# Optimization experiments

Measured on AMD Instinct MI355X. Metric: run time of the kernel, lower is better.

The kernel has to match this reference:

```python
import jax, jax.numpy as jnp
import numpy as np

N_HEAD, D_MODEL, D_K, D_V = 16, 1024, 64, 64
B, S = 2, 2048


def setup_inputs() -> dict:
    key = jax.random.key(0)
    ks = jax.random.split(key, 8)
    xn = lambda k, shp: jax.random.normal(k, shp, dtype=jnp.float32)
    # xavier-normal-ish init for projection params
    std_qk = float(np.sqrt(2.0 / (D_MODEL + D_K)))
    std_v = float(np.sqrt(2.0 / (D_MODEL + D_V)))
    std_p = float(np.sqrt(2.0 / (N_HEAD * D_V + D_MODEL)))
    return {
        "q": xn(ks[0], (B, S, D_MODEL)),
        "k": xn(ks[1], (B, S, D_MODEL)),
        "v": xn(ks[2], (B, S, D_MODEL)),
        "w_qs": xn(ks[3], (N_HEAD, D_MODEL, D_K)) * std_qk,
        "w_ks": xn(ks[4], (N_HEAD, D_MODEL, D_K)) * std_qk,
        "w_vs": xn(ks[5], (N_HEAD, D_MODEL, D_V)) * std_v,
        "proj_w": xn(ks[6], (D_MODEL, N_HEAD * D_V)) * std_p,  # torch Linear weight (out, in)
        "proj_b": jnp.zeros((D_MODEL,), dtype=jnp.float32),
    }


def reference(q, k, v, w_qs, w_ks, w_vs, proj_w, proj_b):
    b, len_q, d_model = q.shape
    len_k = k.shape[1]
    temper = jnp.sqrt(jnp.asarray(d_model, q.dtype))  # NOTE: sqrt(d_model), not sqrt(d_k)
    # per-head projections (head-major, matching q.repeat(n_head,1,1) layout)
    qs = jnp.einsum('bqd,hdk->hbqk', q, w_qs)  # (H,B,Sq,Dk)
    ks = jnp.einsum('bsd,hdk->hbsk', k, w_ks)
    vs = jnp.einsum('bsd,hdv->hbsv', v, w_vs)
    att = jax.nn.softmax(jnp.einsum('hbqk,hbsk->hbqs', qs, ks) / temper, axis=-1)
    # dropout is identity in eval mode
    out = jnp.einsum('hbqs,hbsv->hbqv', att, vs)  # (H,B,Sq,Dv)
    # concat heads along feature dim in head order -> (B,Sq,H*Dv)
    out = jnp.transpose(out, (1, 2, 0, 3)).reshape(b, len_q, -1)
    out = out @ proj_w.T + proj_b
    attns = att.reshape(-1, len_q, len_k)  # (H*B, Sq, Sk) as in original
    return out, attns
```

## Files before the change

kernel.cpp:

```cpp
#include <hip/hip_runtime.h>
#include <hip/hip_bf16.h>
#include <math.h>


typedef __attribute__((ext_vector_type(8))) short short8;
typedef __attribute__((ext_vector_type(4))) float f32x4;
typedef __attribute__((ext_vector_type(4))) unsigned short ushort4v;

#define MFMA16(a, b, c) __builtin_amdgcn_mfma_f32_16x16x32_bf16(a, b, c, 0, 0, 0)
#define EXP2F(x) __builtin_amdgcn_exp2f(x)
#define LOG2F(x) __builtin_amdgcn_logf(x)

#define TILE_BARRIER(N) \
  asm volatile("s_waitcnt vmcnt(" #N ")\n\ts_barrier" ::: "memory")

static __device__ __forceinline__ unsigned short f2bf(float x) {
  unsigned int u = __float_as_uint(x);
  u += 0x7fffu + ((u >> 16) & 1u);
  return (unsigned short)(u >> 16);
}
static __device__ __forceinline__ unsigned int pack2bf(float a, float b) {
  return (unsigned int)f2bf(a) | ((unsigned int)f2bf(b) << 16);
}

static __device__ __forceinline__ void gload16(const unsigned short* g, unsigned short* l) {
  __builtin_amdgcn_global_load_lds(
      (const __attribute__((address_space(1))) unsigned int*)g,
      (__attribute__((address_space(3))) unsigned int*)l, 16, 0, 0);
}

__global__ void k_cvt_all(const float* __restrict__ q, const float* __restrict__ k,
                          const float* __restrict__ v, const float* __restrict__ pw,
                          unsigned short* __restrict__ qb, unsigned short* __restrict__ kb,
                          unsigned short* __restrict__ vb, unsigned short* __restrict__ pwb) {
  const int i = blockIdx.x * blockDim.x + threadIdx.x;
  const int N1 = 1048576;
  const float* s;
  unsigned short* d;
  int off;
  if (i < N1) { s = q; d = qb; off = i; }
  else if (i < 2 * N1) { s = k; d = kb; off = i - N1; }
  else if (i < 3 * N1) { s = v; d = vb; off = i - 2 * N1; }
  else { s = pw; d = pwb; off = i - 3 * N1; }
  float4 vv = reinterpret_cast<const float4*>(s)[off];
  ushort4v o;
  o.x = f2bf(vv.x); o.y = f2bf(vv.y); o.z = f2bf(vv.z); o.w = f2bf(vv.w);
  reinterpret_cast<ushort4v*>(d)[off] = o;
}

__global__ __launch_bounds__(256) void k_wt2(
    const float* __restrict__ s0, const float* __restrict__ s1, const float* __restrict__ s2,
    unsigned short* __restrict__ d0, unsigned short* __restrict__ d1,
    unsigned short* __restrict__ d2) {
  __shared__ float t[64][65];
  const int z = blockIdx.z;
  const float* __restrict__ s = (z == 0) ? s0 : ((z == 1) ? s1 : s2);
  unsigned short* __restrict__ d = (z == 0) ? d0 : ((z == 1) ? d1 : d2);
  const float wscale = (z == 0) ? 0.04508422002778011f : 1.0f;
  const int tid = threadIdx.x;
  const int h = blockIdx.y;
  const int dd0 = blockIdx.x * 64;
  const float* sp = s + ((size_t)h << 16);
  unsigned short* dp = d + ((size_t)h << 16);
#pragma unroll
  for (int it = 0; it < 16; ++it) {
    int dd = it * 4 + (tid >> 6);
    t[dd][tid & 63] = sp[(size_t)(dd0 + dd) * 64 + (tid & 63)];
  }
  __syncthreads();
#pragma unroll
  for (int it = 0; it < 16; ++it) {
    int kk = it * 4 + (tid >> 6);
    int dd = tid & 63;
    dp[(size_t)kk * 1024 + dd0 + dd] = f2bf(t[dd][kk] * wscale);
  }
}

__global__ __launch_bounds__(256, 3) void k_proj(
    const unsigned short* __restrict__ qb, const unsigned short* __restrict__ kb,
    const unsigned short* __restrict__ vb,
    const unsigned short* __restrict__ wqt, const unsigned short* __restrict__ wkt,
    const unsigned short* __restrict__ wvt,
    unsigned short* __restrict__ qs, unsigned short* __restrict__ ks,
    unsigned short* __restrict__ vst) {
  __shared__ unsigned short lA[2][4][128][8];
  __shared__ unsigned short lB[2][4][128][8];

  const int mode = blockIdx.z;
  const unsigned short* __restrict__ A = (mode == 0) ? qb : ((mode == 1) ? kb : vb);
  const unsigned short* __restrict__ W = (mode == 0) ? wqt : ((mode == 1) ? wkt : wvt);

  const int tid = threadIdx.x;
  const int wv = tid >> 6, lane = tid & 63, lq = lane & 15, g = lane >> 4;
  const int wr = wv >> 1, wc = wv & 1;
  const int m0 = blockIdx.x * 128;
  const int n0 = blockIdx.y * 128;

  const int rowm = tid & 127, kg = tid >> 7;
  const unsigned short* srcA = A + (size_t)(m0 + rowm) * 1024 + kg * 8;
  const unsigned short* srcB = W + (size_t)(n0 + rowm) * 1024 + kg * 8;
  unsigned short* dstA = &lA[0][0][0][0] + tid * 8;
  unsigned short* dstB = &lB[0][0][0][0] + tid * 8;

#define STAGE(bf, kc)                                       \
  do {                                                      \
    gload16(srcA + (kc), dstA + (bf)*4096);                 \
    gload16(srcA + (kc) + 16, dstA + (bf)*4096 + 2048);     \
    gload16(srcB + (kc), dstB + (bf)*4096);                 \
    gload16(srcB + (kc) + 16, dstB + (bf)*4096 + 2048);     \
  } while (0)

  f32x4 acc[4][4];
#pragma unroll
  for (int i = 0; i < 4; ++i)
#pragma unroll
    for (int j = 0; j < 4; ++j) acc[i][j] = (f32x4){0.f, 0.f, 0.f, 0.f};

  STAGE(0, 0);
  __syncthreads();
  for (int t = 0; t < 32; ++t) {
    const int buf = t & 1;
    if (t < 31) STAGE(buf ^ 1, (t + 1) * 32);
    short8 a[4], b[4];
#pragma unroll
    for (int i = 0; i < 4; ++i)
      a[i] = *reinterpret_cast<const short8*>(&lA[buf][g][wr * 64 + i * 16 + lq][0]);
#pragma unroll
    for (int j = 0; j < 4; ++j)
      b[j] = *reinterpret_cast<const short8*>(&lB[buf][g][wc * 64 + j * 16 + lq][0]);
#pragma unroll
    for (int i = 0; i < 4; ++i)
#pragma unroll
      for (int j = 0; j < 4; ++j) acc[i][j] = MFMA16(a[i], b[j], acc[i][j]);
    __syncthreads();
  }
#undef STAGE

#pragma unroll
  for (int i = 0; i < 4; ++i) {
#pragma unroll
    for (int j = 0; j < 4; ++j) {
      const int n = n0 + wc * 64 + j * 16 + lq;
      const int h = n >> 6, dk = n & 63;
#pragma unroll
      for (int r = 0; r < 4; ++r) {
        const int m = m0 + wr * 64 + i * 16 + g * 4 + r;
        const int b_ = m >> 11, sq = m & 2047;
        const unsigned short val = f2bf(acc[i][j][r]);
        if (mode == 0)
          qs[(((size_t)h * 2 + b_) * 2048 + sq) * 64 + dk] = val;
        else if (mode == 1)
          ks[(((size_t)h * 2 + b_) * 2048 + sq) * 64 + dk] = val;
        else
          vst[(((size_t)h * 2 + b_) * 64 + dk) * 2048 + sq] = val;
      }
    }
  }
}

__global__ __launch_bounds__(256, 2) void k_attn1(
    const unsigned short* __restrict__ qs, const unsigned short* __restrict__ ks,
    float* __restrict__ cf) {
  __shared__ unsigned short lk[2][4096];

  const int tid = threadIdx.x;
  const int wv = tid >> 6, lane = tid & 63, lq = lane & 15, g = lane >> 4;
  const int bid = blockIdx.x;
  const int xcd = bid & 7, j = bid >> 3;
  const int hb = xcd * 4 + (j & 3);
  const int qblk = j >> 2;
  const int q0 = qblk * 128 + wv * 32;

  const unsigned short* __restrict__ Q = qs + (size_t)hb * 2048 * 64;
  const unsigned short* __restrict__ K = ks + (size_t)hb * 2048 * 64;

  short8 bq[2][2];
#pragma unroll
  for (int s = 0; s < 2; ++s) {
    const size_t qr = (size_t)(q0 + s * 16 + lq) * 64;
    bq[s][0] = *reinterpret_cast<const short8*>(Q + qr + g * 8);
    bq[s][1] = *reinterpret_cast<const short8*>(Q + qr + 32 + g * 8);
  }

  const int srow = tid >> 3;
  const int scg = (tid & 7) ^ (srow & 7);
  const unsigned short* Ks0 = K + (size_t)srow * 64 + scg * 8;
  const unsigned short* Ks1 = K + (size_t)(srow + 32) * 64 + scg * 8;

#define STAGE_K(bf, kt0)                                   \
  do {                                                     \
    gload16(Ks0 + (size_t)(kt0) * 64, &lk[bf][tid * 8]);   \
    gload16(Ks1 + (size_t)(kt0) * 64, &lk[bf][(tid + 256) * 8]); \
  } while (0)

  float lrun[2] = {0.f, 0.f};
  STAGE_K(0, 0);
  TILE_BARRIER(0);
  for (int t = 0; t < 32; ++t) {
    const int buf = t & 1;
    if (t < 31) STAGE_K(buf ^ 1, (t + 1) * 64);
#pragma unroll
    for (int sub = 0; sub < 4; ++sub) {
      const int row = sub * 16 + lq;
      const int c0 = g ^ (row & 7);
      const unsigned short* lp = &lk[buf][row * 64];
      short8 ka0 = *reinterpret_cast<const short8*>(lp + c0 * 8);
      short8 ka1 = *reinterpret_cast<const short8*>(lp + (c0 ^ 4) * 8);
#pragma unroll
      for (int s = 0; s < 2; ++s) {
        f32x4 sa = (f32x4){0.f, 0.f, 0.f, 0.f};
        sa = MFMA16(ka0, bq[s][0], sa);
        sa = MFMA16(ka1, bq[s][1], sa);
        lrun[s] += (EXP2F(sa[0]) + EXP2F(sa[1])) + (EXP2F(sa[2]) + EXP2F(sa[3]));
      }
    }
    TILE_BARRIER(0);
  }
#pragma unroll
  for (int s = 0; s < 2; ++s) {
    float lc = lrun[s] + __shfl_xor(lrun[s], 16);
    lc += __shfl_xor(lc, 32);
    if (g == 0) cf[hb * 2048 + q0 + s * 16 + lq] = LOG2F(lc);
  }
#undef STAGE_K
}

__global__ __launch_bounds__(256, 2) void k_attn2(
    const unsigned short* __restrict__ qs, const unsigned short* __restrict__ ks,
    const unsigned short* __restrict__ vst, const float* __restrict__ cf,
    float* __restrict__ attns, unsigned short* __restrict__ att_out) {
  __shared__ unsigned short lk[2][4096];
  __shared__ unsigned short lv[2][4096];
  __shared__ unsigned char pscr[4][2][2048];

  const int tid = threadIdx.x;
  const int wv = tid >> 6, lane = tid & 63, lq = lane & 15, g = lane >> 4;
  const int bid = blockIdx.x;
  const int xcd = bid & 7, j = bid >> 3;
  const int hb = xcd * 4 + (j & 3);
  const int qblk = j >> 2;
  const int q0 = qblk * 128 + wv * 32;

  const unsigned short* __restrict__ Q = qs + (size_t)hb * 2048 * 64;
  const unsigned short* __restrict__ K = ks + (size_t)hb * 2048 * 64;
  const unsigned short* __restrict__ V = vst + (size_t)hb * 64 * 2048;

  short8 bq[2][2];
  float cfin[2];
#pragma unroll
  for (int s = 0; s < 2; ++s) {
    const size_t qr = (size_t)(q0 + s * 16 + lq) * 64;
    bq[s][0] = *reinterpret_cast<const short8*>(Q + qr + g * 8);
    bq[s][1] = *reinterpret_cast<const short8*>(Q + qr + 32 + g * 8);
    cfin[s] = cf[hb * 2048 + q0 + s * 16 + lq];
  }

  const int srow = tid >> 3;
  const int scg = (tid & 7) ^ (srow & 7);
  const unsigned short* Ks0 = K + (size_t)srow * 64 + scg * 8;
  const unsigned short* Ks1 = K + (size_t)(srow + 32) * 64 + scg * 8;
  const unsigned short* Vs0 = V + (size_t)srow * 2048 + scg * 8;
  const unsigned short* Vs1 = V + (size_t)(srow + 32) * 2048 + scg * 8;

#define STAGE_K(bf, kt0)                                   \
  do {                                                     \
    gload16(Ks0 + (size_t)(kt0) * 64, &lk[bf][tid * 8]);   \
    gload16(Ks1 + (size_t)(kt0) * 64, &lk[bf][(tid + 256) * 8]); \
  } while (0)
#define STAGE_V(bf, kt0)                                   \
  do {                                                     \
    gload16(Vs0 + (kt0), &lv[bf][tid * 8]);                \
    gload16(Vs1 + (kt0), &lv[bf][(tid + 256) * 8]);        \
  } while (0)

  f32x4 oacc[2][4];
#pragma unroll
  for (int s = 0; s < 2; ++s)
#pragma unroll
    for (int db = 0; db < 4; ++db) oacc[s][db] = (f32x4){0.f, 0.f, 0.f, 0.f};

  float* __restrict__ atile = attns + ((size_t)hb * 2048 + q0) * 2048;
  unsigned char* __restrict__ P0 = &pscr[wv][0][0];
  unsigned char* __restrict__ P1 = &pscr[wv][1][0];

  STAGE_K(0, 0);
  STAGE_V(0, 0);
  TILE_BARRIER(0);
  for (int t = 0; t < 32; ++t) {
    const int buf = t & 1;
    if (t < 31) {
      STAGE_K(buf ^ 1, (t + 1) * 64);
      STAGE_V(buf ^ 1, (t + 1) * 64);
    }
#pragma unroll
    for (int sub = 0; sub < 4; ++sub) {
      const int row = sub * 16 + lq;
      const int c0 = g ^ (row & 7);
      const unsigned short* lp = &lk[buf][row * 64];
      short8 ka0 = *reinterpret_cast<const short8*>(lp + c0 * 8);
      short8 ka1 = *reinterpret_cast<const short8*>(lp + (c0 ^ 4) * 8);
      const int cw = ((sub * 2 + (g >> 1)) ^ (lq & 7)) * 16 + (g & 1) * 8;
#pragma unroll
      for (int s = 0; s < 2; ++s) {
        f32x4 sa = (f32x4){0.f, 0.f, 0.f, 0.f};
        sa = MFMA16(ka0, bq[s][0], sa);
        sa = MFMA16(ka1, bq[s][1], sa);
        uint2 pr;
        pr.x = pack2bf(EXP2F(sa[0] - cfin[s]), EXP2F(sa[1] - cfin[s]));
        pr.y = pack2bf(EXP2F(sa[2] - cfin[s]), EXP2F(sa[3] - cfin[s]));
        *reinterpret_cast<uint2*>((s ? P1 : P0) + lq * 128 + cw) = pr;
      }
    }
#pragma unroll
    for (int s = 0; s < 2; ++s) {
      const unsigned char* Ps = s ? P1 : P0;
#pragma unroll
      for (int st = 0; st < 4; ++st) {
        const int rr = st * 4 + g;
        const int cr = ((lq >> 1) ^ (rr & 7)) * 16 + (lq & 1) * 8;
        const uint2 w = *reinterpret_cast<const uint2*>(Ps + rr * 128 + cr);
        f32x4 f4;
        f4[0] = __uint_as_float(w.x << 16);
        f4[1] = __uint_as_float(w.x & 0xffff0000u);
        f4[2] = __uint_as_float(w.y << 16);
        f4[3] = __uint_as_float(w.y & 0xffff0000u);
        float* dst = atile + (size_t)(s * 16 + rr) * 2048 + t * 64 + lq * 4;
        __builtin_nontemporal_store(f4, reinterpret_cast<f32x4*>(dst));
      }
    }
#pragma unroll
    for (int ch = 0; ch < 2; ++ch) {
      const int cp = ((ch * 4 + g) ^ (lq & 7)) * 16;
      short8 pb0 = *reinterpret_cast<const short8*>(P0 + lq * 128 + cp);
      short8 pb1 = *reinterpret_cast<const short8*>(P1 + lq * 128 + cp);
#pragma unroll
      for (int db = 0; db < 4; ++db) {
        const int row = db * 16 + lq;
        const int cv = (ch * 4 + g) ^ (row & 7);
        short8 va = *reinterpret_cast<const short8*>(&lv[buf][row * 64 + cv * 8]);
        oacc[0][db] = MFMA16(va, pb0, oacc[0][db]);
        oacc[1][db] = MFMA16(va, pb1, oacc[1][db]);
      }
    }
    if (t < 31) TILE_BARRIER(8);
  }

  const int h = hb >> 1, b_ = hb & 1;
#pragma unroll
  for (int s = 0; s < 2; ++s) {
    unsigned short* __restrict__ aob =
        att_out + ((size_t)(b_ * 2048 + q0 + s * 16 + lq)) * 1024 + h * 64;
#pragma unroll
    for (int db = 0; db < 4; ++db)
#pragma unroll
      for (int r = 0; r < 4; ++r)
        aob[db * 16 + g * 4 + r] = f2bf(oacc[s][db][r]);
  }
#undef STAGE_K
#undef STAGE_V
}

__global__ __launch_bounds__(256, 2) void k_oproj(
    const unsigned short* __restrict__ ao, const unsigned short* __restrict__ pw,
    const float* __restrict__ pb, float* __restrict__ out) {
  __shared__ unsigned short lA[2][4][64][8];
  __shared__ unsigned short lB[2][4][128][8];

  const int tid = threadIdx.x;
  const int wv = tid >> 6, lane = tid & 63, lq = lane & 15, g = lane >> 4;
  const int wr = wv >> 1, wc = wv & 1;
  const int m0 = blockIdx.x * 64;
  const int n0 = blockIdx.y * 128;

  const int rowa = tid & 63, kga = tid >> 6;
  const unsigned short* srcA = ao + (size_t)(m0 + rowa) * 1024 + kga * 8;
  unsigned short* dstA = &lA[0][0][0][0] + tid * 8;
  const int rowb = tid & 127, kgb = tid >> 7;
  const unsigned short* srcB = pw + (size_t)(n0 + rowb) * 1024 + kgb * 8;
  unsigned short* dstB = &lB[0][0][0][0] + tid * 8;

#define STAGE(bf, kc)                                       \
  do {                                                      \
    gload16(srcA + (kc), dstA + (bf)*2048);                 \
    gload16(srcB + (kc), dstB + (bf)*4096);                 \
    gload16(srcB + (kc) + 16, dstB + (bf)*4096 + 2048);     \
  } while (0)

  f32x4 acc[2][4];
#pragma unroll
  for (int i = 0; i < 2; ++i)
#pragma unroll
    for (int j = 0; j < 4; ++j) acc[i][j] = (f32x4){0.f, 0.f, 0.f, 0.f};

  STAGE(0, 0);
  __syncthreads();
  for (int t = 0; t < 32; ++t) {
    const int buf = t & 1;
    if (t < 31) STAGE(buf ^ 1, (t + 1) * 32);
    short8 a[2], b[4];
#pragma unroll
    for (int i = 0; i < 2; ++i)
      a[i] = *reinterpret_cast<const short8*>(&lA[buf][g][wr * 32 + i * 16 + lq][0]);
#pragma unroll
    for (int j = 0; j < 4; ++j)
      b[j] = *reinterpret_cast<const short8*>(&lB[buf][g][wc * 64 + j * 16 + lq][0]);
#pragma unroll
    for (int i = 0; i < 2; ++i)
#pragma unroll
      for (int j = 0; j < 4; ++j) acc[i][j] = MFMA16(a[i], b[j], acc[i][j]);
    __syncthreads();
  }
#undef STAGE

#pragma unroll
  for (int i = 0; i < 2; ++i) {
#pragma unroll
    for (int j = 0; j < 4; ++j) {
      const int n = n0 + wc * 64 + j * 16 + lq;
      const float bias = pb[n];
#pragma unroll
      for (int r = 0; r < 4; ++r) {
        const int m = m0 + wr * 32 + i * 16 + g * 4 + r;
        out[(size_t)m * 1024 + n] = acc[i][j][r] + bias;
      }
    }
  }
}

extern "C" void kernel_launch(void* const* d_in, const int* in_sizes, int n_in,
                              void* d_out, int out_size, void* d_ws, size_t ws_size,
                              hipStream_t stream) {
  const float* q = (const float*)d_in[0];
  const float* k = (const float*)d_in[1];
  const float* v = (const float*)d_in[2];
  const float* w_qs = (const float*)d_in[3];
  const float* w_ks = (const float*)d_in[4];
  const float* w_vs = (const float*)d_in[5];
  const float* proj_w = (const float*)d_in[6];
  const float* proj_b = (const float*)d_in[7];

  float* out = (float*)d_out;
  float* attns = out + (size_t)2 * 2048 * 1024;

  char* ws = (char*)d_ws;
  unsigned short* qb = (unsigned short*)(ws + ((size_t)0 << 20));
  unsigned short* kb = (unsigned short*)(ws + ((size_t)8 << 20));
  unsigned short* vb = (unsigned short*)(ws + ((size_t)16 << 20));
  unsigned short* wqt = (unsigned short*)(ws + ((size_t)24 << 20));
  unsigned short* wkt = (unsigned short*)(ws + ((size_t)26 << 20));
  unsigned short* wvt = (unsigned short*)(ws + ((size_t)28 << 20));
  unsigned short* pwb = (unsigned short*)(ws + ((size_t)30 << 20));
  unsigned short* qsb = (unsigned short*)(ws + ((size_t)32 << 20));
  unsigned short* ksb = (unsigned short*)(ws + ((size_t)40 << 20));
  unsigned short* vstb = (unsigned short*)(ws + ((size_t)48 << 20));
  unsigned short* aob = (unsigned short*)(ws + ((size_t)56 << 20));
  float* cfb = (float*)(ws + ((size_t)72 << 20));

  k_cvt_all<<<13312, 256, 0, stream>>>(q, k, v, proj_w, qb, kb, vb, pwb);
  k_wt2<<<dim3(16, 16, 3), 256, 0, stream>>>(w_qs, w_ks, w_vs, wqt, wkt, wvt);

  k_proj<<<dim3(32, 8, 3), 256, 0, stream>>>(qb, kb, vb, wqt, wkt, wvt, qsb, ksb, vstb);
  k_attn1<<<dim3(512), 256, 0, stream>>>(qsb, ksb, cfb);
  k_attn2<<<dim3(512), 256, 0, stream>>>(qsb, ksb, vstb, cfb, attns, aob);
  k_oproj<<<dim3(64, 8), 256, 0, stream>>>(aob, pwb, proj_b, out);
}
```

Measured before the change: 263.7 us.

## Batch attention-probability stores into 256-column flushes for full-line writes

The per-wave P scratch grows from one 64-column tile to four tiles (32 rows x 256 columns). Every four key tiles, a FLUSH lambda writes the buffered probabilities out to the fp32 attns matrix. Each wave now stores 1 KB contiguous row segments instead of scattered 256-byte pieces, which is meant to make the dominant attns write stream coalesce better. In exchange, LDS use rises to 64 KB per block, so launch bounds drop to one block per SIMD group and occupancy falls. The barrier waitcnt values also change, which could serialise the loads more.

```diff
diff --git a/kernel.cpp b/kernel.cpp
--- a/kernel.cpp
+++ b/kernel.cpp
@@ -225,13 +225,13 @@
 #undef STAGE_K
 }
 
-__global__ __launch_bounds__(256, 2) void k_attn2(
+__global__ __launch_bounds__(256, 1) void k_attn2(
     const unsigned short* __restrict__ qs, const unsigned short* __restrict__ ks,
     const unsigned short* __restrict__ vst, const float* __restrict__ cf,
     float* __restrict__ attns, unsigned short* __restrict__ att_out) {
   __shared__ unsigned short lk[2][4096];
   __shared__ unsigned short lv[2][4096];
-  __shared__ unsigned char pscr[4][2][2048];
+  __shared__ unsigned char pscr[4][32][512];
 
   const int tid = threadIdx.x;
   const int wv = tid >> 6, lane = tid & 63, lq = lane & 15, g = lane >> 4;
@@ -280,18 +280,36 @@
     for (int db = 0; db < 4; ++db) oacc[s][db] = (f32x4){0.f, 0.f, 0.f, 0.f};
 
   float* __restrict__ atile = attns + ((size_t)hb * 2048 + q0) * 2048;
-  unsigned char* __restrict__ P0 = &pscr[wv][0][0];
-  unsigned char* __restrict__ P1 = &pscr[wv][1][0];
+  unsigned char* __restrict__ Pw = &pscr[wv][0][0];
+
+  auto FLUSH = [&](int bb) {
+    const int tb_ = lane >> 4, cc_ = (lane >> 1) & 7, hf_ = lane & 1;
+#pragma unroll 8
+    for (int jj = 0; jj < 32; ++jj) {
+      const int ph_ = tb_ * 8 + (cc_ ^ (jj & 7));
+      const uint2 w_ = *reinterpret_cast<const uint2*>(
+          Pw + jj * 512 + ph_ * 16 + hf_ * 8);
+      f32x4 f4_;
+      f4_[0] = __uint_as_float(w_.x << 16);
+      f4_[1] = __uint_as_float(w_.x & 0xffff0000u);
+      f4_[2] = __uint_as_float(w_.y << 16);
+      f4_[3] = __uint_as_float(w_.y & 0xffff0000u);
+      float* dst_ = atile + (size_t)jj * 2048 + bb * 256 + lane * 4;
+      __builtin_nontemporal_store(f4_, reinterpret_cast<f32x4*>(dst_));
+    }
+  };
 
   STAGE_K(0, 0);
   STAGE_V(0, 0);
   TILE_BARRIER(0);
   for (int t = 0; t < 32; ++t) {
     const int buf = t & 1;
+    const int i = t & 3;
     if (t < 31) {
       STAGE_K(buf ^ 1, (t + 1) * 64);
       STAGE_V(buf ^ 1, (t + 1) * 64);
     }
+    if (i == 0 && t > 0) FLUSH((t >> 2) - 1);
 #pragma unroll
     for (int sub = 0; sub < 4; ++sub) {
       const int row = sub * 16 + lq;
@@ -299,7 +317,7 @@
       const unsigned short* lp = &lk[buf][row * 64];
       short8 ka0 = *reinterpret_cast<const short8*>(lp + c0 * 8);
       short8 ka1 = *reinterpret_cast<const short8*>(lp + (c0 ^ 4) * 8);
-      const int cw = ((sub * 2 + (g >> 1)) ^ (lq & 7)) * 16 + (g & 1) * 8;
+      const int off = (i * 8 + ((sub * 2 + (g >> 1)) ^ (lq & 7))) * 16 + (g & 1) * 8;
 #pragma unroll
       for (int s = 0; s < 2; ++s) {
         f32x4 sa = (f32x4){0.f, 0.f, 0.f, 0.f};
@@ -308,31 +326,14 @@
         uint2 pr;
         pr.x = pack2bf(EXP2F(sa[0] - cfin[s]), EXP2F(sa[1] - cfin[s]));
         pr.y = pack2bf(EXP2F(sa[2] - cfin[s]), EXP2F(sa[3] - cfin[s]));
-        *reinterpret_cast<uint2*>((s ? P1 : P0) + lq * 128 + cw) = pr;
+        *reinterpret_cast<uint2*>(Pw + (s * 16 + lq) * 512 + off) = pr;
       }
     }
 #pragma unroll
-    for (int s = 0; s < 2; ++s) {
-      const unsigned char* Ps = s ? P1 : P0;
-#pragma unroll
-      for (int st = 0; st < 4; ++st) {
-        const int rr = st * 4 + g;
-        const int cr = ((lq >> 1) ^ (rr & 7)) * 16 + (lq & 1) * 8;
-        const uint2 w = *reinterpret_cast<const uint2*>(Ps + rr * 128 + cr);
-        f32x4 f4;
-        f4[0] = __uint_as_float(w.x << 16);
-        f4[1] = __uint_as_float(w.x & 0xffff0000u);
-        f4[2] = __uint_as_float(w.y << 16);
-        f4[3] = __uint_as_float(w.y & 0xffff0000u);
-        float* dst = atile + (size_t)(s * 16 + rr) * 2048 + t * 64 + lq * 4;
-        __builtin_nontemporal_store(f4, reinterpret_cast<f32x4*>(dst));
-      }
-    }
-#pragma unroll
     for (int ch = 0; ch < 2; ++ch) {
-      const int cp = ((ch * 4 + g) ^ (lq & 7)) * 16;
-      short8 pb0 = *reinterpret_cast<const short8*>(P0 + lq * 128 + cp);
-      short8 pb1 = *reinterpret_cast<const short8*>(P1 + lq * 128 + cp);
+      const int cp = (i * 8 + ((ch * 4 + g) ^ (lq & 7))) * 16;
+      short8 pb0 = *reinterpret_cast<const short8*>(Pw + lq * 512 + cp);
+      short8 pb1 = *reinterpret_cast<const short8*>(Pw + (16 + lq) * 512 + cp);
 #pragma unroll
       for (int db = 0; db < 4; ++db) {
         const int row = db * 16 + lq;
@@ -342,8 +343,12 @@
         oacc[1][db] = MFMA16(va, pb1, oacc[1][db]);
       }
     }
-    if (t < 31) TILE_BARRIER(8);
-  }
+    if (t < 31) {
+      if (i == 0 && t > 0) { TILE_BARRIER(32); }
+      else { TILE_BARRIER(0); }
+    }
+  }
+  FLUSH(7);
 
   const int h = hb >> 1, b_ = hb & 1;
 #pragma unroll
```

Result: slower. 310.7 us (+17.8%).

## Split attn2 waves into stats and output roles, halve attn1 grid, fuse preprocessing kernels

Applied to the files above, without the earlier changes.

Merges the conversion and weight-transpose kernels into one launch. Cuts the row-statistics kernel to half its grid, so it computes log-sum-exp only for half of the query blocks. In the attention kernel, waves 2-3 now compute their own log-sum-exp during a first pass over the 32 key tiles, while waves 0-1 already produce probabilities using the precomputed statistics. In a second pass the roles swap, so stats work overlaps output work inside one block. The kernel now does 64 tile iterations instead of 32, adds more K/V loads and uses different barrier wait counts depending on wave role, which risks imbalance and extra memory traffic.

```diff
diff --git a/kernel.cpp b/kernel.cpp
--- a/kernel.cpp
+++ b/kernel.cpp
@@ -29,37 +29,39 @@
       (__attribute__((address_space(3))) unsigned int*)l, 16, 0, 0);
 }
 
-__global__ void k_cvt_all(const float* __restrict__ q, const float* __restrict__ k,
-                          const float* __restrict__ v, const float* __restrict__ pw,
-                          unsigned short* __restrict__ qb, unsigned short* __restrict__ kb,
-                          unsigned short* __restrict__ vb, unsigned short* __restrict__ pwb) {
-  const int i = blockIdx.x * blockDim.x + threadIdx.x;
-  const int N1 = 1048576;
-  const float* s;
-  unsigned short* d;
-  int off;
-  if (i < N1) { s = q; d = qb; off = i; }
-  else if (i < 2 * N1) { s = k; d = kb; off = i - N1; }
-  else if (i < 3 * N1) { s = v; d = vb; off = i - 2 * N1; }
-  else { s = pw; d = pwb; off = i - 3 * N1; }
-  float4 vv = reinterpret_cast<const float4*>(s)[off];
-  ushort4v o;
-  o.x = f2bf(vv.x); o.y = f2bf(vv.y); o.z = f2bf(vv.z); o.w = f2bf(vv.w);
-  reinterpret_cast<ushort4v*>(d)[off] = o;
-}
-
-__global__ __launch_bounds__(256) void k_wt2(
-    const float* __restrict__ s0, const float* __restrict__ s1, const float* __restrict__ s2,
-    unsigned short* __restrict__ d0, unsigned short* __restrict__ d1,
-    unsigned short* __restrict__ d2) {
+__global__ __launch_bounds__(256) void k_pre(
+    const float* __restrict__ q, const float* __restrict__ k,
+    const float* __restrict__ v, const float* __restrict__ pw,
+    unsigned short* __restrict__ qb, unsigned short* __restrict__ kb,
+    unsigned short* __restrict__ vb, unsigned short* __restrict__ pwb,
+    const float* __restrict__ s0, const float* __restrict__ s1,
+    const float* __restrict__ s2, unsigned short* __restrict__ d0,
+    unsigned short* __restrict__ d1, unsigned short* __restrict__ d2) {
   __shared__ float t[64][65];
-  const int z = blockIdx.z;
+  const int bid = blockIdx.x;
+  const int tid = threadIdx.x;
+  if (bid < 13312) {
+    const int i = bid * 256 + tid;
+    const int N1 = 1048576;
+    const float* s;
+    unsigned short* d;
+    int off;
+    if (i < N1) { s = q; d = qb; off = i; }
+    else if (i < 2 * N1) { s = k; d = kb; off = i - N1; }
+    else if (i < 3 * N1) { s = v; d = vb; off = i - 2 * N1; }
+    else { s = pw; d = pwb; off = i - 3 * N1; }
+    float4 vv = reinterpret_cast<const float4*>(s)[off];
+    ushort4v o;
+    o.x = f2bf(vv.x); o.y = f2bf(vv.y); o.z = f2bf(vv.z); o.w = f2bf(vv.w);
+    reinterpret_cast<ushort4v*>(d)[off] = o;
+    return;
+  }
+  const int b2 = bid - 13312;
+  const int z = b2 >> 8, rem = b2 & 255;
+  const int h = rem >> 4, dd0 = (rem & 15) * 64;
   const float* __restrict__ s = (z == 0) ? s0 : ((z == 1) ? s1 : s2);
   unsigned short* __restrict__ d = (z == 0) ? d0 : ((z == 1) ? d1 : d2);
   const float wscale = (z == 0) ? 0.04508422002778011f : 1.0f;
-  const int tid = threadIdx.x;
-  const int h = blockIdx.y;
-  const int dd0 = blockIdx.x * 64;
   const float* sp = s + ((size_t)h << 16);
   unsigned short* dp = d + ((size_t)h << 16);
 #pragma unroll
@@ -166,10 +168,11 @@
   const int tid = threadIdx.x;
   const int wv = tid >> 6, lane = tid & 63, lq = lane & 15, g = lane >> 4;
   const int bid = blockIdx.x;
-  const int xcd = bid & 7, j = bid >> 3;
-  const int hb = xcd * 4 + (j & 3);
-  const int qblk = j >> 2;
-  const int q0 = qblk * 128 + wv * 32;
+  const int xcd = bid & 7, m = bid >> 3;
+  const int hb = xcd * 4 + (m & 3);
+  const int qi = m >> 2;
+  const int qpair = 2 * qi + (wv >> 1);
+  const int q0 = qpair * 128 + (wv & 1) * 32;
 
   const unsigned short* __restrict__ Q = qs + (size_t)hb * 2048 * 64;
   const unsigned short* __restrict__ K = ks + (size_t)hb * 2048 * 64;
@@ -240,19 +243,23 @@
   const int hb = xcd * 4 + (j & 3);
   const int qblk = j >> 2;
   const int q0 = qblk * 128 + wv * 32;
+  const bool isA = (wv < 2);
 
   const unsigned short* __restrict__ Q = qs + (size_t)hb * 2048 * 64;
   const unsigned short* __restrict__ K = ks + (size_t)hb * 2048 * 64;
   const unsigned short* __restrict__ V = vst + (size_t)hb * 64 * 2048;
 
   short8 bq[2][2];
-  float cfin[2];
+  float cfin[2] = {0.f, 0.f};
 #pragma unroll
   for (int s = 0; s < 2; ++s) {
     const size_t qr = (size_t)(q0 + s * 16 + lq) * 64;
     bq[s][0] = *reinterpret_cast<const short8*>(Q + qr + g * 8);
     bq[s][1] = *reinterpret_cast<const short8*>(Q + qr + 32 + g * 8);
-    cfin[s] = cf[hb * 2048 + q0 + s * 16 + lq];
+  }
+  if (isA) {
+#pragma unroll
+    for (int s = 0; s < 2; ++s) cfin[s] = cf[hb * 2048 + q0 + s * 16 + lq];
   }
 
   const int srow = tid >> 3;
@@ -278,6 +285,7 @@
   for (int s = 0; s < 2; ++s)
 #pragma unroll
     for (int db = 0; db < 4; ++db) oacc[s][db] = (f32x4){0.f, 0.f, 0.f, 0.f};
+  float lrun[2] = {0.f, 0.f};
 
   float* __restrict__ atile = attns + ((size_t)hb * 2048 + q0) * 2048;
   unsigned char* __restrict__ P0 = &pscr[wv][0][0];
@@ -286,63 +294,95 @@
   STAGE_K(0, 0);
   STAGE_V(0, 0);
   TILE_BARRIER(0);
-  for (int t = 0; t < 32; ++t) {
-    const int buf = t & 1;
-    if (t < 31) {
-      STAGE_K(buf ^ 1, (t + 1) * 64);
-      STAGE_V(buf ^ 1, (t + 1) * 64);
+  for (int p = 0; p < 64; ++p) {
+    const int tl = p & 31;
+    const int buf = p & 1;
+    if (p < 63) {
+      const int nt_ = ((p + 1) & 31) * 64;
+      STAGE_K(buf ^ 1, nt_);
+      STAGE_V(buf ^ 1, nt_);
     }
-#pragma unroll
-    for (int sub = 0; sub < 4; ++sub) {
-      const int row = sub * 16 + lq;
-      const int c0 = g ^ (row & 7);
-      const unsigned short* lp = &lk[buf][row * 64];
-      short8 ka0 = *reinterpret_cast<const short8*>(lp + c0 * 8);
-      short8 ka1 = *reinterpret_cast<const short8*>(lp + (c0 ^ 4) * 8);
-      const int cw = ((sub * 2 + (g >> 1)) ^ (lq & 7)) * 16 + (g & 1) * 8;
+    const bool s2 = (isA == (p < 32));
+    if (s2) {
+#pragma unroll
+      for (int sub = 0; sub < 4; ++sub) {
+        const int row = sub * 16 + lq;
+        const int c0 = g ^ (row & 7);
+        const unsigned short* lp = &lk[buf][row * 64];
+        short8 ka0 = *reinterpret_cast<const short8*>(lp + c0 * 8);
+        short8 ka1 = *reinterpret_cast<const short8*>(lp + (c0 ^ 4) * 8);
+        const int cw = ((sub * 2 + (g >> 1)) ^ (lq & 7)) * 16 + (g & 1) * 8;
+#pragma unroll
+        for (int s = 0; s < 2; ++s) {
+          f32x4 sa = (f32x4){0.f, 0.f, 0.f, 0.f};
+          sa = MFMA16(ka0, bq[s][0], sa);
+          sa = MFMA16(ka1, bq[s][1], sa);
+          uint2 pr;
+          pr.x = pack2bf(EXP2F(sa[0] - cfin[s]), EXP2F(sa[1] - cfin[s]));
+          pr.y = pack2bf(EXP2F(sa[2] - cfin[s]), EXP2F(sa[3] - cfin[s]));
+          *reinterpret_cast<uint2*>((s ? P1 : P0) + lq * 128 + cw) = pr;
+        }
+      }
 #pragma unroll
       for (int s = 0; s < 2; ++s) {
-        f32x4 sa = (f32x4){0.f, 0.f, 0.f, 0.f};
-        sa = MFMA16(ka0, bq[s][0], sa);
-        sa = MFMA16(ka1, bq[s][1], sa);
-        uint2 pr;
-        pr.x = pack2bf(EXP2F(sa[0] - cfin[s]), EXP2F(sa[1] - cfin[s]));
-        pr.y = pack2bf(EXP2F(sa[2] - cfin[s]), EXP2F(sa[3] - cfin[s]));
-        *reinterpret_cast<uint2*>((s ? P1 : P0) + lq * 128 + cw) = pr;
+        const unsigned char* Ps = s ? P1 : P0;
+#pragma unroll
+        for (int st = 0; st < 4; ++st) {
+          const int rr = st * 4 + g;
+          const int cr = ((lq >> 1) ^ (rr & 7)) * 16 + (lq & 1) * 8;
+          const uint2 w = *reinterpret_cast<const uint2*>(Ps + rr * 128 + cr);
+          f32x4 f4;
+          f4[0] = __uint_as_float(w.x << 16);
+          f4[1] = __uint_as_float(w.x & 0xffff0000u);
+          f4[2] = __uint_as_float(w.y << 16);
+          f4[3] = __uint_as_float(w.y & 0xffff0000u);
+          float* dst = atile + (size_t)(s * 16 + rr) * 2048 + tl * 64 + lq * 4;
+          __builtin_nontemporal_store(f4, reinterpret_cast<f32x4*>(dst));
+        }
+      }
+#pragma unroll
+      for (int ch = 0; ch < 2; ++ch) {
+        const int cp = ((ch * 4 + g) ^ (lq & 7)) * 16;
+        short8 pb0 = *reinterpret_cast<const short8*>(P0 + lq * 128 + cp);
+        short8 pb1 = *reinterpret_cast<const short8*>(P1 + lq * 128 + cp);
+#pragma unroll
+        for (int db = 0; db < 4; ++db) {
+          const int row = db * 16 + lq;
+          const int cv = (ch * 4 + g) ^ (row & 7);
+          short8 va = *reinterpret_cast<const short8*>(&lv[buf][row * 64 + cv * 8]);
+          oacc[0][db] = MFMA16(va, pb0, oacc[0][db]);
+          oacc[1][db] = MFMA16(va, pb1, oacc[1][db]);
+        }
+      }
+    } else if (!isA) {
+#pragma unroll
+      for (int sub = 0; sub < 4; ++sub) {
+        const int row = sub * 16 + lq;
+        const int c0 = g ^ (row & 7);
+        const unsigned short* lp = &lk[buf][row * 64];
+        short8 ka0 = *reinterpret_cast<const short8*>(lp + c0 * 8);
+        short8 ka1 = *reinterpret_cast<const short8*>(lp + (c0 ^ 4) * 8);
+#pragma unroll
+        for (int s = 0; s < 2; ++s) {
+          f32x4 sa = (f32x4){0.f, 0.f, 0.f, 0.f};
+          sa = MFMA16(ka0, bq[s][0], sa);
+          sa = MFMA16(ka1, bq[s][1], sa);
+          lrun[s] += (EXP2F(sa[0]) + EXP2F(sa[1])) + (EXP2F(sa[2]) + EXP2F(sa[3]));
+        }
+      }
+      if (p == 31) {
+#pragma unroll
+        for (int s = 0; s < 2; ++s) {
+          float lc = lrun[s] + __shfl_xor(lrun[s], 16);
+          lc += __shfl_xor(lc, 32);
+          cfin[s] = LOG2F(lc);
+        }
       }
     }
-#pragma unroll
-    for (int s = 0; s < 2; ++s) {
-      const unsigned char* Ps = s ? P1 : P0;
-#pragma unroll
-      for (int st = 0; st < 4; ++st) {
-        const int rr = st * 4 + g;
-        const int cr = ((lq >> 1) ^ (rr & 7)) * 16 + (lq & 1) * 8;
-        const uint2 w = *reinterpret_cast<const uint2*>(Ps + rr * 128 + cr);
-        f32x4 f4;
-        f4[0] = __uint_as_float(w.x << 16);
-        f4[1] = __uint_as_float(w.x & 0xffff0000u);
-        f4[2] = __uint_as_float(w.y << 16);
-        f4[3] = __uint_as_float(w.y & 0xffff0000u);
-        float* dst = atile + (size_t)(s * 16 + rr) * 2048 + t * 64 + lq * 4;
-        __builtin_nontemporal_store(f4, reinterpret_cast<f32x4*>(dst));
-      }
+    if (p < 63) {
+      if (s2) { TILE_BARRIER(8); }
+      else    { TILE_BARRIER(0); }
     }
-#pragma unroll
-    for (int ch = 0; ch < 2; ++ch) {
-      const int cp = ((ch * 4 + g) ^ (lq & 7)) * 16;
-      short8 pb0 = *reinterpret_cast<const short8*>(P0 + lq * 128 + cp);
-      short8 pb1 = *reinterpret_cast<const short8*>(P1 + lq * 128 + cp);
-#pragma unroll
-      for (int db = 0; db < 4; ++db) {
-        const int row = db * 16 + lq;
-        const int cv = (ch * 4 + g) ^ (row & 7);
-        short8 va = *reinterpret_cast<const short8*>(&lv[buf][row * 64 + cv * 8]);
-        oacc[0][db] = MFMA16(va, pb0, oacc[0][db]);
-        oacc[1][db] = MFMA16(va, pb1, oacc[1][db]);
-      }
-    }
-    if (t < 31) TILE_BARRIER(8);
   }
 
   const int h = hb >> 1, b_ = hb & 1;
@@ -456,11 +496,10 @@
   unsigned short* aob = (unsigned short*)(ws + ((size_t)56 << 20));
   float* cfb = (float*)(ws + ((size_t)72 << 20));
 
-  k_cvt_all<<<13312, 256, 0, stream>>>(q, k, v, proj_w, qb, kb, vb, pwb);
-  k_wt2<<<dim3(16, 16, 3), 256, 0, stream>>>(w_qs, w_ks, w_vs, wqt, wkt, wvt);
-
+  k_pre<<<14080, 256, 0, stream>>>(q, k, v, proj_w, qb, kb, vb, pwb,
+                                   w_qs, w_ks, w_vs, wqt, wkt, wvt);
   k_proj<<<dim3(32, 8, 3), 256, 0, stream>>>(qb, kb, vb, wqt, wkt, wvt, qsb, ksb, vstb);
-  k_attn1<<<dim3(512), 256, 0, stream>>>(qsb, ksb, cfb);
+  k_attn1<<<dim3(256), 256, 0, stream>>>(qsb, ksb, cfb);
   k_attn2<<<dim3(512), 256, 0, stream>>>(qsb, ksb, vstb, cfb, attns, aob);
   k_oproj<<<dim3(64, 8), 256, 0, stream>>>(aob, pwb, proj_b, out);
 }
```

Result: faster. 256.7 us (-2.7%).
